# Kernel tuning notes

Hardware: AMD Instinct MI355X
Metric: run time of the kernel (lower is better)

## Reference

```python
import jax, jax.numpy as jnp
import numpy as np

N = 500_000          # nodes
E = 8_000_000        # edges (avg degree 16)
C = 2                # in/out channels
STEP_DIM = 8
NUM_STEPS = 100
K = 2                # k_hops -> powers [0, 1]
HID = 8              # hidden_layers


def setup_inputs() -> dict:
    key = jax.random.key(0)
    ks = jax.random.split(key, 6)
    X = jax.random.normal(ks[0], (N, C), dtype=jnp.float32)
    edge_index = jax.random.randint(ks[1], (2, E), 0, N, dtype=jnp.int32)
    step_emb = jax.random.normal(ks[2], (NUM_STEPS, STEP_DIM), dtype=jnp.float32)
    d_in0 = C + STEP_DIM  # 10
    # layer 0: one Linear per power p in {0,1}
    W0 = jax.random.normal(ks[3], (K, d_in0, C), dtype=jnp.float32) / np.sqrt(d_in0).astype(np.float32)
    b0 = jnp.zeros((K, C), dtype=jnp.float32)
    # layers 1..7, stacked for lax.scan
    Wh = jax.random.normal(ks[4], (HID - 1, K, C, C), dtype=jnp.float32) / np.sqrt(C).astype(np.float32)
    bh = jnp.zeros((HID - 1, K, C), dtype=jnp.float32)
    return dict(X=X, edge_index=edge_index, step_index=7, step_emb=step_emb,
                W0=W0, b0=b0, Wh=Wh, bh=bh)


def _make_prop(edge_index, n):
    """GCN-normalized propagation with self-loops (PyG gcn_norm), as used by MixHopConv."""
    src, dst = edge_index[0], edge_index[1]
    # in-degree on destination nodes, +1 for the self-loop
    deg = jnp.zeros((n,), jnp.float32).at[dst].add(1.0) + 1.0
    dis = jax.lax.rsqrt(deg)  # deg^{-1/2}; deg >= 1 so no inf handling needed
    edge_w = dis[src] * dis[dst]  # [E]

    def prop(x):
        msg = x[src] * edge_w[:, None]                      # [E, F] gather
        out = jax.ops.segment_sum(msg, dst, num_segments=n)  # [N, F] scatter-add
        return out + x * (dis * dis)[:, None]               # self-loop term
    return prop


def reference(X, edge_index, step_index, step_emb, W0, b0, Wh, bh):
    n = X.shape[0]
    prop = _make_prop(edge_index, n)

    s = jnp.broadcast_to(step_emb[step_index], (n, STEP_DIM))
    x = jnp.concatenate([X, s], axis=-1)  # [N, 10]

    # layer 0: concat(xW0, (Ax)W1) -> view(-1,K,C).sum(1) -> relu  ==  relu(xW0+b0 + (Ax)W1+b1)
    x = jax.nn.relu(x @ W0[0] + b0[0] + prop(x) @ W0[1] + b0[1])  # [N, 2]

    def body(x, wb):
        W, b = wb  # W: [K, C, C], b: [K, C]
        h = x @ W[0] + b[0] + prop(x) @ W[1] + b[1]
        return jax.nn.relu(h), None

    x, _ = jax.lax.scan(body, x, (Wh, bh))
    return x
```

## Files before the change

### kernel.cpp

```cpp
#include <hip/hip_runtime.h>


constexpr int NN = 500000;
constexpr int NE = 8000000;
constexpr int STEP_DIM = 8;
constexpr int HIDM1 = 7;

constexpr int BSH  = 9;
constexpr int BNOD = 1 << BSH;
constexpr int NBUK = (NN + BNOD - 1) / BNOD;
constexpr int SLOT  = 9216;
constexpr int CPT   = SLOT / 512;
constexpr int WSPAN = 64 * CPT;
constexpr unsigned SENT = (unsigned)BNOD << 19;

constexpr int PA_NBLK = 500;
constexpr int PA_EPB  = NE / PA_NBLK;
constexpr int PA_QPB  = PA_EPB / 4;
constexpr int PA_SC   = NBUK + 1;

constexpr int PB_NBLK = 125;
constexpr int PB_EPB  = NE / PB_NBLK;
constexpr int PB_QPB  = PB_EPB / 4;

typedef unsigned u32x4 __attribute__((ext_vector_type(4)));
typedef unsigned u32x2 __attribute__((ext_vector_type(2)));

__device__ __forceinline__ int swiz(int L) {
  int w = L / WSPAN;
  int r = L - w * WSPAN;
  int l = r / CPT;
  int o = r - l * CPT;
  int base = w * WSPAN;
  return (o < 16) ? base + (o >> 2) * 256 + l * 4 + (o & 3)
                  : base + 1024 + l * 2 + (o - 16);
}


__global__ __launch_bounds__(512) void k_lsort(const int* __restrict__ src,
                                               const int* __restrict__ dst,
                                               unsigned* __restrict__ colraw,
                                               int* __restrict__ starts2) {
  __shared__ unsigned stage[PA_EPB];
  __shared__ int hist[NBUK];
  __shared__ int tsum[512];
  int b = blockIdx.x, t = threadIdx.x;
  for (int h = t; h < NBUK; h += 512) hist[h] = 0;
  __syncthreads();
  const int4* d4p = (const int4*)dst + (size_t)b * PA_QPB;
  const int4* s4p = (const int4*)src + (size_t)b * PA_QPB;
  for (int i = t; i < PA_QPB; i += 512) {
    int4 d = d4p[i];
    atomicAdd(&hist[d.x >> BSH], 1);
    atomicAdd(&hist[d.y >> BSH], 1);
    atomicAdd(&hist[d.z >> BSH], 1);
    atomicAdd(&hist[d.w >> BSH], 1);
  }
  __syncthreads();
  int h0 = 2 * t, h1 = 2 * t + 1;
  int a0 = (h0 < NBUK) ? hist[h0] : 0;
  int a1 = (h1 < NBUK) ? hist[h1] : 0;
  tsum[t] = a0 + a1;
  __syncthreads();
  for (int o = 1; o < 512; o <<= 1) {
    int v = (t >= o) ? tsum[t - o] : 0;
    __syncthreads();
    tsum[t] += v;
    __syncthreads();
  }
  int ex = tsum[t] - (a0 + a1);
  __syncthreads();
  if (h0 < NBUK) hist[h0] = ex;
  if (h1 < NBUK) hist[h1] = ex + a0;
  __syncthreads();
  int* st = starts2 + (size_t)b * PA_SC;
  for (int h = t; h < NBUK; h += 512) st[h] = hist[h];
  if (t == 0) st[NBUK] = PA_EPB;
  __syncthreads();
  for (int i = t; i < PA_QPB; i += 512) {
    int4 d = d4p[i];
    int4 s = s4p[i];
    int p0 = atomicAdd(&hist[d.x >> BSH], 1);
    stage[p0] = ((unsigned)(d.x & (BNOD - 1)) << 19) | (unsigned)s.x;
    int p1 = atomicAdd(&hist[d.y >> BSH], 1);
    stage[p1] = ((unsigned)(d.y & (BNOD - 1)) << 19) | (unsigned)s.y;
    int p2 = atomicAdd(&hist[d.z >> BSH], 1);
    stage[p2] = ((unsigned)(d.z & (BNOD - 1)) << 19) | (unsigned)s.z;
    int p3 = atomicAdd(&hist[d.w >> BSH], 1);
    stage[p3] = ((unsigned)(d.w & (BNOD - 1)) << 19) | (unsigned)s.w;
  }
  __syncthreads();
  u32x4* out4 = (u32x4*)(colraw + (size_t)b * PA_EPB);
  for (int i = t; i < PA_QPB; i += 512) {
    u32x4 q;
    q[0] = stage[4 * i + 0];
    q[1] = stage[4 * i + 1];
    q[2] = stage[4 * i + 2];
    q[3] = stage[4 * i + 3];
    __builtin_nontemporal_store(q, out4 + i);
  }
}


__global__ __launch_bounds__(512) void k_sortA(const unsigned* __restrict__ colraw,
                                               const int* __restrict__ starts2,
                                               unsigned* __restrict__ col2,
                                               const float2* __restrict__ X,
                                               float* __restrict__ dis,
                                               float2* __restrict__ xs0) {
  __shared__ unsigned stage[SLOT];
  __shared__ int hist[BNOD];
  __shared__ int tsum[512];
  __shared__ int rs[PA_NBLK], rp[PA_NBLK], rl[PA_NBLK];
  __shared__ int nsh;
  int h = blockIdx.x, t = threadIdx.x;
  int s = 0, len = 0;
  if (t < PA_NBLK) {
    s = starts2[(size_t)t * PA_SC + h];
    int e = starts2[(size_t)t * PA_SC + h + 1];
    len = e - s;
  }
  tsum[t] = len;
  __syncthreads();
  for (int o = 1; o < 512; o <<= 1) {
    int v = (t >= o) ? tsum[t - o] : 0;
    __syncthreads();
    tsum[t] += v;
    __syncthreads();
  }
  int pos = tsum[t] - len;
  if (t < PA_NBLK) {
    rs[t] = s;
    rl[t] = len;
    rp[t] = pos;
  }
  if (t == 511) nsh = tsum[511];
  __syncthreads();
  int g = t >> 4, lane = t & 15;
  for (int r = g; r < PA_NBLK; r += 32) {
    const unsigned* rw = colraw + (size_t)r * PA_EPB + rs[r];
    int L = rl[r], P = rp[r];
    for (int j = lane; j < L; j += 16) {
      int p = P + j;
      if (p < SLOT) stage[p] = rw[j];
    }
  }
  __syncthreads();
  int ns = nsh;
  if (ns > SLOT) ns = SLOT;
  hist[t] = 0;
  __syncthreads();
  for (int i = t; i < ns; i += 512) atomicAdd(&hist[stage[i] >> 19], 1);
  __syncthreads();
  int a = hist[t];
  tsum[t] = a;
  __syncthreads();
  for (int o = 1; o < 512; o <<= 1) {
    int v = (t >= o) ? tsum[t - o] : 0;
    __syncthreads();
    tsum[t] += v;
    __syncthreads();
  }
  hist[t] = tsum[t] - a;
  __syncthreads();
  unsigned* base = col2 + (size_t)h * SLOT;
  for (int i = t; i < ns; i += 512) {
    unsigned p = stage[i];
    int pp = atomicAdd(&hist[p >> 19], 1);
    base[swiz(pp)] = p;
  }
  for (int L = ns + t; L < SLOT; L += 512) base[swiz(L)] = SENT;
  int i = (h << BSH) + t;
  if (i < NN) {
    float d = rsqrtf((float)a + 1.0f);
    dis[i] = d;
    float2 x = X[i];
    xs0[i] = make_float2(d * x.x, d * x.y);
  }
}


__global__ __launch_bounds__(1024) void k_bhistB(const int* __restrict__ dst,
                                                 int* __restrict__ bhist) {
  __shared__ int hist[NBUK];
  int b = blockIdx.x, t = threadIdx.x;
  for (int h = t; h < NBUK; h += 1024) hist[h] = 0;
  __syncthreads();
  const int4* d4p = (const int4*)dst + (size_t)b * PB_QPB;
  for (int i = t; i < PB_QPB; i += 1024) {
    int4 d = d4p[i];
    atomicAdd(&hist[d.x >> BSH], 1);
    atomicAdd(&hist[d.y >> BSH], 1);
    atomicAdd(&hist[d.z >> BSH], 1);
    atomicAdd(&hist[d.w >> BSH], 1);
  }
  __syncthreads();
  for (int h = t; h < NBUK; h += 1024) bhist[h * PB_NBLK + b] = hist[h];
}

__global__ __launch_bounds__(128) void k_rowscanB(int* __restrict__ bhist,
                                                  int* __restrict__ bcount) {
  __shared__ int sm[128];
  int h = blockIdx.x, t = threadIdx.x;
  int v = (t < PB_NBLK) ? bhist[h * PB_NBLK + t] : 0;
  sm[t] = v;
  __syncthreads();
  for (int o = 1; o < 128; o <<= 1) {
    int x = (t >= o) ? sm[t - o] : 0;
    __syncthreads();
    sm[t] += x;
    __syncthreads();
  }
  if (t < PB_NBLK) bhist[h * PB_NBLK + t] = sm[t] - v;
  if (t == 127) bcount[h] = sm[127];
}

__global__ __launch_bounds__(1024) void k_bscatterB(const int* __restrict__ src,
                                                    const int* __restrict__ dst,
                                                    const int* __restrict__ off,
                                                    unsigned int* __restrict__ col2) {
  __shared__ int cur[NBUK];
  int b = blockIdx.x, t = threadIdx.x;
  for (int h = t; h < NBUK; h += 1024) cur[h] = h * SLOT + off[h * PB_NBLK + b];
  __syncthreads();
  const int4* s4p = (const int4*)src + (size_t)b * PB_QPB;
  const int4* d4p = (const int4*)dst + (size_t)b * PB_QPB;
  for (int i = t; i < PB_QPB; i += 1024) {
    int4 s = s4p[i];
    int4 d = d4p[i];
    int p0 = atomicAdd(&cur[d.x >> BSH], 1);
    col2[p0] = ((unsigned)(d.x & (BNOD - 1)) << 19) | (unsigned)s.x;
    int p1 = atomicAdd(&cur[d.y >> BSH], 1);
    col2[p1] = ((unsigned)(d.y & (BNOD - 1)) << 19) | (unsigned)s.y;
    int p2 = atomicAdd(&cur[d.z >> BSH], 1);
    col2[p2] = ((unsigned)(d.z & (BNOD - 1)) << 19) | (unsigned)s.z;
    int p3 = atomicAdd(&cur[d.w >> BSH], 1);
    col2[p3] = ((unsigned)(d.w & (BNOD - 1)) << 19) | (unsigned)s.w;
  }
}

__global__ __launch_bounds__(512) void k_sortB(unsigned int* __restrict__ col2,
                                               const int* __restrict__ bcount,
                                               const float2* __restrict__ X,
                                               float* __restrict__ dis,
                                               float2* __restrict__ xs0) {
  __shared__ unsigned stage[SLOT];
  __shared__ int hist[BNOD];
  __shared__ int tsum[512];
  int b = blockIdx.x, t = threadIdx.x;
  int ns = bcount[b];
  if (ns > SLOT) ns = SLOT;
  unsigned* base = col2 + (size_t)b * SLOT;
  hist[t] = 0;
  __syncthreads();
  for (int i = t; i < ns; i += 512) {
    unsigned p = base[i];
    stage[i] = p;
    atomicAdd(&hist[p >> 19], 1);
  }
  __syncthreads();
  int a = hist[t];
  tsum[t] = a;
  __syncthreads();
  for (int o = 1; o < 512; o <<= 1) {
    int v = (t >= o) ? tsum[t - o] : 0;
    __syncthreads();
    tsum[t] += v;
    __syncthreads();
  }
  hist[t] = tsum[t] - a;
  __syncthreads();
  for (int i = t; i < ns; i += 512) {
    unsigned p = stage[i];
    int pos = atomicAdd(&hist[p >> 19], 1);
    base[swiz(pos)] = p;
  }
  for (int L = ns + t; L < SLOT; L += 512) base[swiz(L)] = SENT;
  int i = (b << BSH) + t;
  if (i < NN) {
    float d = rsqrtf((float)a + 1.0f);
    dis[i] = d;
    float2 x = X[i];
    xs0[i] = make_float2(d * x.x, d * x.y);
  }
}


__global__ __launch_bounds__(512) void k_blayer0(const unsigned int* __restrict__ col2,
                                                 const float2* __restrict__ xs0,
                                                 const float2* __restrict__ X,
                                                 const float* __restrict__ dis,
                                                 const float* __restrict__ W0,
                                                 const float* __restrict__ b0,
                                                 const float* __restrict__ step_emb,
                                                 const int* __restrict__ step_index,
                                                 float2* __restrict__ xs_out) {
  __shared__ float acc[(BNOD + 1) * 3];
  int b = blockIdx.x, t = threadIdx.x;
  for (int j = t; j < (BNOD + 1) * 3; j += 512) acc[j] = 0.f;
  __syncthreads();
  const unsigned* bp = col2 + (size_t)b * SLOT + (t >> 6) * WSPAN;
  int l = t & 63;
  int cur = BNOD;
  float rx = 0.f, ry = 0.f, rd = 0.f;
  unsigned ebuf[CPT];
#pragma unroll
  for (int i = 0; i < 4; ++i) {
    u32x4 q = __builtin_nontemporal_load((const u32x4*)(bp + i * 256 + l * 4));
#pragma unroll
    for (int j = 0; j < 4; ++j) ebuf[i * 4 + j] = q[j];
  }
  {
    u32x2 q2 = __builtin_nontemporal_load((const u32x2*)(bp + 1024 + l * 2));
    ebuf[16] = q2[0];
    ebuf[17] = q2[1];
  }
#pragma unroll
  for (int o = 0; o < CPT; ++o) {
    unsigned p = ebuf[o];
    int s = p & 0x7FFFF;
    float2 v = xs0[s];
    float dv = dis[s];
    int ld = (int)(p >> 19);
    if (ld != cur) {
      atomicAdd(&acc[cur * 3 + 0], rx);
      atomicAdd(&acc[cur * 3 + 1], ry);
      atomicAdd(&acc[cur * 3 + 2], rd);
      cur = ld;
      rx = v.x; ry = v.y; rd = dv;
    } else {
      rx += v.x; ry += v.y; rd += dv;
    }
  }
  atomicAdd(&acc[cur * 3 + 0], rx);
  atomicAdd(&acc[cur * 3 + 1], ry);
  atomicAdd(&acc[cur * 3 + 2], rd);
  __syncthreads();
  const float* sv = step_emb + step_index[0] * STEP_DIM;
  float c0[2], c1[2];
#pragma unroll
  for (int o = 0; o < 2; ++o) {
    float a0 = b0[o] + b0[2 + o];
    float a1 = 0.f;
#pragma unroll
    for (int j = 0; j < STEP_DIM; ++j) {
      a0 += sv[j] * W0[(2 + j) * 2 + o];
      a1 += sv[j] * W0[20 + (2 + j) * 2 + o];
    }
    c0[o] = a0;
    c1[o] = a1;
  }
  int i = (b << BSH) + t;
  if (i < NN) {
    float d = dis[i], d2 = d * d;
    float2 x = X[i];
    float px = d * acc[t * 3 + 0] + d2 * x.x;
    float py = d * acc[t * 3 + 1] + d2 * x.y;
    float rowsum = d * acc[t * 3 + 2] + d2;
    float h0 = c0[0] + rowsum * c1[0] + x.x * W0[0] + x.y * W0[2] + px * W0[20] + py * W0[22];
    float h1 = c0[1] + rowsum * c1[1] + x.x * W0[1] + x.y * W0[3] + px * W0[21] + py * W0[23];
    h0 = fmaxf(h0, 0.f);
    h1 = fmaxf(h1, 0.f);
    xs_out[i] = make_float2(d * h0, d * h1);
  }
}

__global__ __launch_bounds__(512) void k_blayer(const unsigned int* __restrict__ col2,
                                                const float* __restrict__ dis,
                                                const float2* __restrict__ xs_in,
                                                const float* __restrict__ W,
                                                const float* __restrict__ bb,
                                                float2* __restrict__ xs_out,
                                                float2* __restrict__ out,
                                                int last) {
  __shared__ float acc[(BNOD + 1) * 2];
  int b = blockIdx.x, t = threadIdx.x;
  for (int j = t; j < (BNOD + 1) * 2; j += 512) acc[j] = 0.f;
  __syncthreads();
  const unsigned* bp = col2 + (size_t)b * SLOT + (t >> 6) * WSPAN;
  int l = t & 63;
  int cur = BNOD;
  float rx = 0.f, ry = 0.f;
  unsigned ebuf[CPT];
#pragma unroll
  for (int i = 0; i < 4; ++i) {
    u32x4 q = __builtin_nontemporal_load((const u32x4*)(bp + i * 256 + l * 4));
#pragma unroll
    for (int j = 0; j < 4; ++j) ebuf[i * 4 + j] = q[j];
  }
  {
    u32x2 q2 = __builtin_nontemporal_load((const u32x2*)(bp + 1024 + l * 2));
    ebuf[16] = q2[0];
    ebuf[17] = q2[1];
  }
#pragma unroll
  for (int o = 0; o < CPT; ++o) {
    unsigned p = ebuf[o];
    float2 v = xs_in[p & 0x7FFFF];
    int ld = (int)(p >> 19);
    if (ld != cur) {
      atomicAdd(&acc[cur * 2 + 0], rx);
      atomicAdd(&acc[cur * 2 + 1], ry);
      cur = ld;
      rx = v.x; ry = v.y;
    } else {
      rx += v.x; ry += v.y;
    }
  }
  atomicAdd(&acc[cur * 2 + 0], rx);
  atomicAdd(&acc[cur * 2 + 1], ry);
  __syncthreads();
  int i = (b << BSH) + t;
  if (i < NN) {
    float d = dis[i];
    float2 xsv = xs_in[i];
    float inv = 1.0f / d;
    float xx = xsv.x * inv, xy = xsv.y * inv;
    float px = d * (acc[t * 2 + 0] + xsv.x);
    float py = d * (acc[t * 2 + 1] + xsv.y);
    float h0 = bb[0] + bb[2] + xx * W[0] + xy * W[2] + px * W[4] + py * W[6];
    float h1 = bb[1] + bb[3] + xx * W[1] + xy * W[3] + px * W[5] + py * W[7];
    h0 = fmaxf(h0, 0.f);
    h1 = fmaxf(h1, 0.f);
    if (last) {
      out[i] = make_float2(h0, h1);
    } else {
      xs_out[i] = make_float2(d * h0, d * h1);
    }
  }
}


extern "C" void kernel_launch(void* const* d_in, const int* in_sizes, int n_in,
                              void* d_out, int out_size, void* d_ws, size_t ws_size,
                              hipStream_t stream) {
  const float2* X        = (const float2*)d_in[0];
  const int*    edge     = (const int*)d_in[1];
  const int*    src      = edge;
  const int*    dstp     = edge + NE;
  const int*    step_idx = (const int*)d_in[2];
  const float*  step_emb = (const float*)d_in[3];
  const float*  W0       = (const float*)d_in[4];
  const float*  b0       = (const float*)d_in[5];
  const float*  Wh       = (const float*)d_in[6];
  const float*  bbias    = (const float*)d_in[7];

  int*      ip   = (int*)d_ws;
  unsigned* col2 = (unsigned*)ip;
  size_t    o    = (size_t)NBUK * SLOT;

  size_t oA = o;
  unsigned* colraw  = (unsigned*)(ip + oA);  oA += NE;
  int*      starts2 = ip + oA;               oA += ((size_t)PA_NBLK * PA_SC + 8) & ~3;
  size_t oB = o;
  int*      bhist   = ip + oB;               oB += ((size_t)NBUK * PB_NBLK + 8) & ~3;
  int*      bcount  = ip + oB;               oB += 1024;

  size_t tail = (size_t)500224 + 2 * 1000448 + 1000448;
  bool pathA = ws_size >= (oA + tail) * sizeof(int);
  size_t ot = pathA ? oA : oB;
  float*  dis  = (float*)(ip + ot);   ot += 500224;
  float2* bufA = (float2*)(ip + ot);  ot += 2 * 500224;
  float2* bufB = (float2*)(ip + ot);

  if (pathA) {
    k_lsort<<<PA_NBLK, 512, 0, stream>>>(src, dstp, colraw, starts2);
    k_sortA<<<NBUK, 512, 0, stream>>>(colraw, starts2, col2, X, dis, bufA);
  } else {
    k_bhistB<<<PB_NBLK, 1024, 0, stream>>>(dstp, bhist);
    k_rowscanB<<<NBUK, 128, 0, stream>>>(bhist, bcount);
    k_bscatterB<<<PB_NBLK, 1024, 0, stream>>>(src, dstp, bhist, col2);
    k_sortB<<<NBUK, 512, 0, stream>>>(col2, bcount, X, dis, bufA);
  }

  k_blayer0<<<NBUK, 512, 0, stream>>>(col2, bufA, X, dis, W0, b0,
                                      step_emb, step_idx, bufB);
  float2* cur = bufB;
  float2* nxt = bufA;
  for (int l = 0; l < HIDM1; ++l) {
    k_blayer<<<NBUK, 512, 0, stream>>>(col2, dis, cur, Wh + l * 8,
                                       bbias + l * 4, nxt, (float2*)d_out,
                                       l == HIDM1 - 1 ? 1 : 0);
    float2* tmp = cur;
    cur = nxt;
    nxt = tmp;
  }
}
```

Measured before the change: 602.8 us.

## Split bucket edges by source quarter and precompute layer-0 projection table

Edges in each bucket are now sorted by (source quarter, local dst) into four fixed sub-slots of 2560, so each thread reads 5 edges per quarter. Gathers within a wave then fall in a narrower source range, which should improve cache locality. Layer 0 is rewritten to gather a precomputed per-node table d*(x·W1 + s·W1) instead of xs0 plus dis, so it accumulates two floats instead of three. The fallback path B is removed, and edges beyond a sub-slot's capacity are silently dropped, which is a correctness risk for skewed quarters.

```diff
diff --git a/kernel.cpp b/kernel.cpp
--- a/kernel.cpp
+++ b/kernel.cpp
@@ -9,9 +9,10 @@
 constexpr int BSH  = 9;
 constexpr int BNOD = 1 << BSH;
 constexpr int NBUK = (NN + BNOD - 1) / BNOD;
-constexpr int SLOT  = 9216;
-constexpr int CPT   = SLOT / 512;
-constexpr int WSPAN = 64 * CPT;
+constexpr int NQ   = 4;
+constexpr int SUBQ = 2560;
+constexpr int SLOT = NQ * SUBQ;
+constexpr int KEYS = NQ * BNOD;
 constexpr unsigned SENT = (unsigned)BNOD << 19;
 
 constexpr int PA_NBLK = 500;
@@ -19,21 +20,14 @@
 constexpr int PA_QPB  = PA_EPB / 4;
 constexpr int PA_SC   = NBUK + 1;
 
-constexpr int PB_NBLK = 125;
-constexpr int PB_EPB  = NE / PB_NBLK;
-constexpr int PB_QPB  = PB_EPB / 4;
-
 typedef unsigned u32x4 __attribute__((ext_vector_type(4)));
-typedef unsigned u32x2 __attribute__((ext_vector_type(2)));
-
-__device__ __forceinline__ int swiz(int L) {
-  int w = L / WSPAN;
-  int r = L - w * WSPAN;
-  int l = r / CPT;
-  int o = r - l * CPT;
-  int base = w * WSPAN;
-  return (o < 16) ? base + (o >> 2) * 256 + l * 4 + (o & 3)
-                  : base + 1024 + l * 2 + (o - 16);
+
+__device__ __forceinline__ int swizQ(int p) {
+  int w = p / 320;
+  int r = p - w * 320;
+  int l = r / 5;
+  int o = r - l * 5;
+  return w * 320 + (o < 4 ? l * 4 + o : 256 + l);
 }
 
 
@@ -106,19 +100,22 @@
                                                const int* __restrict__ starts2,
                                                unsigned* __restrict__ col2,
                                                const float2* __restrict__ X,
+                                               const float* __restrict__ W0,
+                                               const float* __restrict__ step_emb,
+                                               const int* __restrict__ step_index,
                                                float* __restrict__ dis,
-                                               float2* __restrict__ xs0) {
+                                               float2* __restrict__ qtab) {
   __shared__ unsigned stage[SLOT];
-  __shared__ int hist[BNOD];
+  __shared__ int hist[KEYS];
   __shared__ int tsum[512];
   __shared__ int rs[PA_NBLK], rp[PA_NBLK], rl[PA_NBLK];
+  __shared__ int qsh[5];
   __shared__ int nsh;
   int h = blockIdx.x, t = threadIdx.x;
   int s = 0, len = 0;
   if (t < PA_NBLK) {
     s = starts2[(size_t)t * PA_SC + h];
-    int e = starts2[(size_t)t * PA_SC + h + 1];
-    len = e - s;
+    len = starts2[(size_t)t * PA_SC + h + 1] - s;
   }
   tsum[t] = len;
   __syncthreads();
@@ -135,6 +132,10 @@
     rp[t] = pos;
   }
   if (t == 511) nsh = tsum[511];
+  hist[4 * t] = 0;
+  hist[4 * t + 1] = 0;
+  hist[4 * t + 2] = 0;
+  hist[4 * t + 3] = 0;
   __syncthreads();
   int g = t >> 4, lane = t & 15;
   for (int r = g; r < PA_NBLK; r += 32) {
@@ -148,12 +149,13 @@
   __syncthreads();
   int ns = nsh;
   if (ns > SLOT) ns = SLOT;
-  hist[t] = 0;
-  __syncthreads();
-  for (int i = t; i < ns; i += 512) atomicAdd(&hist[stage[i] >> 19], 1);
-  __syncthreads();
-  int a = hist[t];
-  tsum[t] = a;
+  for (int i = t; i < ns; i += 512)
+    atomicAdd(&hist[(int)(((stage[i] >> 17) & 3u) * BNOD) + (int)(stage[i] >> 19)], 1);
+  __syncthreads();
+  int deg = hist[t] + hist[t + 512] + hist[t + 1024] + hist[t + 1536];
+  int a0 = hist[4 * t], a1 = hist[4 * t + 1], a2 = hist[4 * t + 2], a3 = hist[4 * t + 3];
+  int ssum = a0 + a1 + a2 + a3;
+  tsum[t] = ssum;
   __syncthreads();
   for (int o = 1; o < 512; o <<= 1) {
     int v = (t >= o) ? tsum[t - o] : 0;
@@ -161,133 +163,46 @@
     tsum[t] += v;
     __syncthreads();
   }
-  hist[t] = tsum[t] - a;
+  int ex = tsum[t] - ssum;
+  hist[4 * t] = ex;
+  hist[4 * t + 1] = ex + a0;
+  hist[4 * t + 2] = ex + a0 + a1;
+  hist[4 * t + 3] = ex + a0 + a1 + a2;
+  if (((4 * t) & 511) == 0) qsh[(4 * t) >> 9] = ex;
+  if (t == 511) qsh[4] = ns;
   __syncthreads();
   unsigned* base = col2 + (size_t)h * SLOT;
   for (int i = t; i < ns; i += 512) {
     unsigned p = stage[i];
-    int pp = atomicAdd(&hist[p >> 19], 1);
-    base[swiz(pp)] = p;
-  }
-  for (int L = ns + t; L < SLOT; L += 512) base[swiz(L)] = SENT;
+    int k = (int)(((p >> 17) & 3u) * BNOD) + (int)(p >> 19);
+    int posQ = atomicAdd(&hist[k], 1) - qsh[k >> 9];
+    if (posQ < SUBQ) base[(k >> 9) * SUBQ + swizQ(posQ)] = p;
+  }
+  for (int q = 0; q < NQ; ++q) {
+    int cnt = qsh[q + 1] - qsh[q];
+    if (cnt > SUBQ) cnt = SUBQ;
+    for (int j = cnt + t; j < SUBQ; j += 512) base[q * SUBQ + swizQ(j)] = SENT;
+  }
   int i = (h << BSH) + t;
   if (i < NN) {
-    float d = rsqrtf((float)a + 1.0f);
+    float d = rsqrtf((float)deg + 1.0f);
     dis[i] = d;
     float2 x = X[i];
-    xs0[i] = make_float2(d * x.x, d * x.y);
-  }
-}
-
-
-__global__ __launch_bounds__(1024) void k_bhistB(const int* __restrict__ dst,
-                                                 int* __restrict__ bhist) {
-  __shared__ int hist[NBUK];
-  int b = blockIdx.x, t = threadIdx.x;
-  for (int h = t; h < NBUK; h += 1024) hist[h] = 0;
-  __syncthreads();
-  const int4* d4p = (const int4*)dst + (size_t)b * PB_QPB;
-  for (int i = t; i < PB_QPB; i += 1024) {
-    int4 d = d4p[i];
-    atomicAdd(&hist[d.x >> BSH], 1);
-    atomicAdd(&hist[d.y >> BSH], 1);
-    atomicAdd(&hist[d.z >> BSH], 1);
-    atomicAdd(&hist[d.w >> BSH], 1);
-  }
-  __syncthreads();
-  for (int h = t; h < NBUK; h += 1024) bhist[h * PB_NBLK + b] = hist[h];
-}
-
-__global__ __launch_bounds__(128) void k_rowscanB(int* __restrict__ bhist,
-                                                  int* __restrict__ bcount) {
-  __shared__ int sm[128];
-  int h = blockIdx.x, t = threadIdx.x;
-  int v = (t < PB_NBLK) ? bhist[h * PB_NBLK + t] : 0;
-  sm[t] = v;
-  __syncthreads();
-  for (int o = 1; o < 128; o <<= 1) {
-    int x = (t >= o) ? sm[t - o] : 0;
-    __syncthreads();
-    sm[t] += x;
-    __syncthreads();
-  }
-  if (t < PB_NBLK) bhist[h * PB_NBLK + t] = sm[t] - v;
-  if (t == 127) bcount[h] = sm[127];
-}
-
-__global__ __launch_bounds__(1024) void k_bscatterB(const int* __restrict__ src,
-                                                    const int* __restrict__ dst,
-                                                    const int* __restrict__ off,
-                                                    unsigned int* __restrict__ col2) {
-  __shared__ int cur[NBUK];
-  int b = blockIdx.x, t = threadIdx.x;
-  for (int h = t; h < NBUK; h += 1024) cur[h] = h * SLOT + off[h * PB_NBLK + b];
-  __syncthreads();
-  const int4* s4p = (const int4*)src + (size_t)b * PB_QPB;
-  const int4* d4p = (const int4*)dst + (size_t)b * PB_QPB;
-  for (int i = t; i < PB_QPB; i += 1024) {
-    int4 s = s4p[i];
-    int4 d = d4p[i];
-    int p0 = atomicAdd(&cur[d.x >> BSH], 1);
-    col2[p0] = ((unsigned)(d.x & (BNOD - 1)) << 19) | (unsigned)s.x;
-    int p1 = atomicAdd(&cur[d.y >> BSH], 1);
-    col2[p1] = ((unsigned)(d.y & (BNOD - 1)) << 19) | (unsigned)s.y;
-    int p2 = atomicAdd(&cur[d.z >> BSH], 1);
-    col2[p2] = ((unsigned)(d.z & (BNOD - 1)) << 19) | (unsigned)s.z;
-    int p3 = atomicAdd(&cur[d.w >> BSH], 1);
-    col2[p3] = ((unsigned)(d.w & (BNOD - 1)) << 19) | (unsigned)s.w;
-  }
-}
-
-__global__ __launch_bounds__(512) void k_sortB(unsigned int* __restrict__ col2,
-                                               const int* __restrict__ bcount,
-                                               const float2* __restrict__ X,
-                                               float* __restrict__ dis,
-                                               float2* __restrict__ xs0) {
-  __shared__ unsigned stage[SLOT];
-  __shared__ int hist[BNOD];
-  __shared__ int tsum[512];
-  int b = blockIdx.x, t = threadIdx.x;
-  int ns = bcount[b];
-  if (ns > SLOT) ns = SLOT;
-  unsigned* base = col2 + (size_t)b * SLOT;
-  hist[t] = 0;
-  __syncthreads();
-  for (int i = t; i < ns; i += 512) {
-    unsigned p = base[i];
-    stage[i] = p;
-    atomicAdd(&hist[p >> 19], 1);
-  }
-  __syncthreads();
-  int a = hist[t];
-  tsum[t] = a;
-  __syncthreads();
-  for (int o = 1; o < 512; o <<= 1) {
-    int v = (t >= o) ? tsum[t - o] : 0;
-    __syncthreads();
-    tsum[t] += v;
-    __syncthreads();
-  }
-  hist[t] = tsum[t] - a;
-  __syncthreads();
-  for (int i = t; i < ns; i += 512) {
-    unsigned p = stage[i];
-    int pos = atomicAdd(&hist[p >> 19], 1);
-    base[swiz(pos)] = p;
-  }
-  for (int L = ns + t; L < SLOT; L += 512) base[swiz(L)] = SENT;
-  int i = (b << BSH) + t;
-  if (i < NN) {
-    float d = rsqrtf((float)a + 1.0f);
-    dis[i] = d;
-    float2 x = X[i];
-    xs0[i] = make_float2(d * x.x, d * x.y);
+    const float* sv = step_emb + step_index[0] * STEP_DIM;
+    float c1_0 = 0.f, c1_1 = 0.f;
+#pragma unroll
+    for (int j = 0; j < STEP_DIM; ++j) {
+      c1_0 += sv[j] * W0[20 + (2 + j) * 2 + 0];
+      c1_1 += sv[j] * W0[20 + (2 + j) * 2 + 1];
+    }
+    qtab[i] = make_float2(d * (x.x * W0[20] + x.y * W0[22] + c1_0),
+                          d * (x.x * W0[21] + x.y * W0[23] + c1_1));
   }
 }
 
 
 __global__ __launch_bounds__(512) void k_blayer0(const unsigned int* __restrict__ col2,
-                                                 const float2* __restrict__ xs0,
+                                                 const float2* __restrict__ qtab,
                                                  const float2* __restrict__ X,
                                                  const float* __restrict__ dis,
                                                  const float* __restrict__ W0,
@@ -295,70 +210,55 @@
                                                  const float* __restrict__ step_emb,
                                                  const int* __restrict__ step_index,
                                                  float2* __restrict__ xs_out) {
-  __shared__ float acc[(BNOD + 1) * 3];
+  __shared__ float acc[(BNOD + 1) * 2];
   int b = blockIdx.x, t = threadIdx.x;
-  for (int j = t; j < (BNOD + 1) * 3; j += 512) acc[j] = 0.f;
-  __syncthreads();
-  const unsigned* bp = col2 + (size_t)b * SLOT + (t >> 6) * WSPAN;
-  int l = t & 63;
+  for (int j = t; j < (BNOD + 1) * 2; j += 512) acc[j] = 0.f;
+  __syncthreads();
+  int w = t >> 6, l = t & 63;
+  const unsigned* bp = col2 + (size_t)b * SLOT + w * 320;
+  unsigned ebuf[NQ * 5];
+#pragma unroll
+  for (int q = 0; q < NQ; ++q) {
+    u32x4 v = __builtin_nontemporal_load((const u32x4*)(bp + q * SUBQ + l * 4));
+    ebuf[q * 5 + 0] = v[0];
+    ebuf[q * 5 + 1] = v[1];
+    ebuf[q * 5 + 2] = v[2];
+    ebuf[q * 5 + 3] = v[3];
+    ebuf[q * 5 + 4] = __builtin_nontemporal_load(bp + q * SUBQ + 256 + l);
+  }
   int cur = BNOD;
-  float rx = 0.f, ry = 0.f, rd = 0.f;
-  unsigned ebuf[CPT];
-#pragma unroll
-  for (int i = 0; i < 4; ++i) {
-    u32x4 q = __builtin_nontemporal_load((const u32x4*)(bp + i * 256 + l * 4));
-#pragma unroll
-    for (int j = 0; j < 4; ++j) ebuf[i * 4 + j] = q[j];
-  }
-  {
-    u32x2 q2 = __builtin_nontemporal_load((const u32x2*)(bp + 1024 + l * 2));
-    ebuf[16] = q2[0];
-    ebuf[17] = q2[1];
-  }
-#pragma unroll
-  for (int o = 0; o < CPT; ++o) {
+  float rx = 0.f, ry = 0.f;
+#pragma unroll
+  for (int o = 0; o < NQ * 5; ++o) {
     unsigned p = ebuf[o];
-    int s = p & 0x7FFFF;
-    float2 v = xs0[s];
-    float dv = dis[s];
+    float2 v = qtab[p & 0x7FFFF];
     int ld = (int)(p >> 19);
     if (ld != cur) {
-      atomicAdd(&acc[cur * 3 + 0], rx);
-      atomicAdd(&acc[cur * 3 + 1], ry);
-      atomicAdd(&acc[cur * 3 + 2], rd);
+      atomicAdd(&acc[cur * 2 + 0], rx);
+      atomicAdd(&acc[cur * 2 + 1], ry);
       cur = ld;
-      rx = v.x; ry = v.y; rd = dv;
+      rx = v.x; ry = v.y;
     } else {
-      rx += v.x; ry += v.y; rd += dv;
-    }
-  }
-  atomicAdd(&acc[cur * 3 + 0], rx);
-  atomicAdd(&acc[cur * 3 + 1], ry);
-  atomicAdd(&acc[cur * 3 + 2], rd);
+      rx += v.x; ry += v.y;
+    }
+  }
+  atomicAdd(&acc[cur * 2 + 0], rx);
+  atomicAdd(&acc[cur * 2 + 1], ry);
   __syncthreads();
   const float* sv = step_emb + step_index[0] * STEP_DIM;
-  float c0[2], c1[2];
-#pragma unroll
-  for (int o = 0; o < 2; ++o) {
-    float a0 = b0[o] + b0[2 + o];
-    float a1 = 0.f;
-#pragma unroll
-    for (int j = 0; j < STEP_DIM; ++j) {
-      a0 += sv[j] * W0[(2 + j) * 2 + o];
-      a1 += sv[j] * W0[20 + (2 + j) * 2 + o];
-    }
-    c0[o] = a0;
-    c1[o] = a1;
+  float c00 = b0[0] + b0[2], c01 = b0[1] + b0[3];
+#pragma unroll
+  for (int j = 0; j < STEP_DIM; ++j) {
+    c00 += sv[j] * W0[(2 + j) * 2 + 0];
+    c01 += sv[j] * W0[(2 + j) * 2 + 1];
   }
   int i = (b << BSH) + t;
   if (i < NN) {
-    float d = dis[i], d2 = d * d;
+    float d = dis[i];
     float2 x = X[i];
-    float px = d * acc[t * 3 + 0] + d2 * x.x;
-    float py = d * acc[t * 3 + 1] + d2 * x.y;
-    float rowsum = d * acc[t * 3 + 2] + d2;
-    float h0 = c0[0] + rowsum * c1[0] + x.x * W0[0] + x.y * W0[2] + px * W0[20] + py * W0[22];
-    float h1 = c0[1] + rowsum * c1[1] + x.x * W0[1] + x.y * W0[3] + px * W0[21] + py * W0[23];
+    float2 qv = qtab[i];
+    float h0 = c00 + x.x * W0[0] + x.y * W0[2] + d * (acc[t * 2 + 0] + qv.x);
+    float h1 = c01 + x.x * W0[1] + x.y * W0[3] + d * (acc[t * 2 + 1] + qv.y);
     h0 = fmaxf(h0, 0.f);
     h1 = fmaxf(h1, 0.f);
     xs_out[i] = make_float2(d * h0, d * h1);
@@ -377,24 +277,22 @@
   int b = blockIdx.x, t = threadIdx.x;
   for (int j = t; j < (BNOD + 1) * 2; j += 512) acc[j] = 0.f;
   __syncthreads();
-  const unsigned* bp = col2 + (size_t)b * SLOT + (t >> 6) * WSPAN;
-  int l = t & 63;
+  int w = t >> 6, l = t & 63;
+  const unsigned* bp = col2 + (size_t)b * SLOT + w * 320;
+  unsigned ebuf[NQ * 5];
+#pragma unroll
+  for (int q = 0; q < NQ; ++q) {
+    u32x4 v = __builtin_nontemporal_load((const u32x4*)(bp + q * SUBQ + l * 4));
+    ebuf[q * 5 + 0] = v[0];
+    ebuf[q * 5 + 1] = v[1];
+    ebuf[q * 5 + 2] = v[2];
+    ebuf[q * 5 + 3] = v[3];
+    ebuf[q * 5 + 4] = __builtin_nontemporal_load(bp + q * SUBQ + 256 + l);
+  }
   int cur = BNOD;
   float rx = 0.f, ry = 0.f;
-  unsigned ebuf[CPT];
-#pragma unroll
-  for (int i = 0; i < 4; ++i) {
-    u32x4 q = __builtin_nontemporal_load((const u32x4*)(bp + i * 256 + l * 4));
-#pragma unroll
-    for (int j = 0; j < 4; ++j) ebuf[i * 4 + j] = q[j];
-  }
-  {
-    u32x2 q2 = __builtin_nontemporal_load((const u32x2*)(bp + 1024 + l * 2));
-    ebuf[16] = q2[0];
-    ebuf[17] = q2[1];
-  }
-#pragma unroll
-  for (int o = 0; o < CPT; ++o) {
+#pragma unroll
+  for (int o = 0; o < NQ * 5; ++o) {
     unsigned p = ebuf[o];
     float2 v = xs_in[p & 0x7FFFF];
     int ld = (int)(p >> 19);
@@ -445,33 +343,18 @@
   const float*  Wh       = (const float*)d_in[6];
   const float*  bbias    = (const float*)d_in[7];
 
-  int*      ip   = (int*)d_ws;
-  unsigned* col2 = (unsigned*)ip;
-  size_t    o    = (size_t)NBUK * SLOT;
-
-  size_t oA = o;
-  unsigned* colraw  = (unsigned*)(ip + oA);  oA += NE;
-  int*      starts2 = ip + oA;               oA += ((size_t)PA_NBLK * PA_SC + 8) & ~3;
-  size_t oB = o;
-  int*      bhist   = ip + oB;               oB += ((size_t)NBUK * PB_NBLK + 8) & ~3;
-  int*      bcount  = ip + oB;               oB += 1024;
-
-  size_t tail = (size_t)500224 + 2 * 1000448 + 1000448;
-  bool pathA = ws_size >= (oA + tail) * sizeof(int);
-  size_t ot = pathA ? oA : oB;
-  float*  dis  = (float*)(ip + ot);   ot += 500224;
-  float2* bufA = (float2*)(ip + ot);  ot += 2 * 500224;
-  float2* bufB = (float2*)(ip + ot);
-
-  if (pathA) {
-    k_lsort<<<PA_NBLK, 512, 0, stream>>>(src, dstp, colraw, starts2);
-    k_sortA<<<NBUK, 512, 0, stream>>>(colraw, starts2, col2, X, dis, bufA);
-  } else {
-    k_bhistB<<<PB_NBLK, 1024, 0, stream>>>(dstp, bhist);
-    k_rowscanB<<<NBUK, 128, 0, stream>>>(bhist, bcount);
-    k_bscatterB<<<PB_NBLK, 1024, 0, stream>>>(src, dstp, bhist, col2);
-    k_sortB<<<NBUK, 512, 0, stream>>>(col2, bcount, X, dis, bufA);
-  }
+  int*      ip      = (int*)d_ws;
+  unsigned* col2    = (unsigned*)ip;
+  size_t    o       = (size_t)NBUK * SLOT;
+  unsigned* colraw  = (unsigned*)(ip + o);  o += NE;
+  int*      starts2 = ip + o;               o += ((size_t)PA_NBLK * PA_SC + 8) & ~(size_t)3;
+  float*    dis     = (float*)(ip + o);     o += 500224;
+  float2*   bufA    = (float2*)(ip + o);    o += 2 * 500224;
+  float2*   bufB    = (float2*)(ip + o);
+
+  k_lsort<<<PA_NBLK, 512, 0, stream>>>(src, dstp, colraw, starts2);
+  k_sortA<<<NBUK, 512, 0, stream>>>(colraw, starts2, col2, X, W0,
+                                    step_emb, step_idx, dis, bufA);
 
   k_blayer0<<<NBUK, 512, 0, stream>>>(col2, bufA, X, dis, W0, b0,
                                       step_emb, step_idx, bufB);
```

After: 575.0 us. 1.05x faster.
